# Performance work log

Hardware: AMD Instinct MI355X
Metric: run time of the kernel (lower is better)

## Reference

```python
import jax, jax.numpy as jnp
import numpy as np

N_NODES = 50000
N_EDGES = 800000
N_GRAPHS = 256
IN_CH = 128
HID = 128
OUT_CH = 10
BN_EPS = 1e-5


def setup_inputs() -> dict:
    key = jax.random.key(0)
    ks = jax.random.split(key, 32)
    x = jax.random.normal(ks[0], (N_NODES, IN_CH), dtype=jnp.float32)
    edge_index = jax.random.randint(ks[1], (2, N_EDGES), 0, N_NODES)
    batch = jnp.sort(jax.random.randint(ks[2], (N_NODES,), 0, N_GRAPHS))

    def lin(k, fan_in, fan_out):
        return (jax.random.normal(k, (fan_in, fan_out), dtype=jnp.float32)
                * np.float32(1.0 / np.sqrt(fan_in)))

    inp = {"x": x, "edge_index": edge_index, "batch": batch}
    dims = [(IN_CH, HID), (HID, HID), (HID, HID)]
    for i, (fi, fo) in enumerate(dims):
        inp[f"W{i}"] = lin(ks[3 + i], fi, fo)
        inp[f"b{i}"] = jnp.zeros((fo,), jnp.float32)
        inp[f"g{i}"] = jnp.ones((fo,), jnp.float32)
        inp[f"be{i}"] = jnp.zeros((fo,), jnp.float32)
    inp["lin1_w"] = lin(ks[10], 2 * HID, HID)
    inp["lin1_b"] = jnp.zeros((HID,), jnp.float32)
    inp["lin2_w"] = lin(ks[11], HID, OUT_CH)
    inp["lin2_b"] = jnp.zeros((OUT_CH,), jnp.float32)
    return inp


def _gcn_conv(x, W, b, src, dst):
    # PyG GCNConv: h = X W; add self-loops; symmetric D^-1/2 (A+I) D^-1/2 aggregation.
    h = x @ W  # [N, F]
    loops = jnp.arange(N_NODES)
    s = jnp.concatenate([src, loops])
    d = jnp.concatenate([dst, loops])
    deg = jax.ops.segment_sum(jnp.ones_like(d, jnp.float32), d, num_segments=N_NODES)
    dinv = jnp.where(deg > 0, jax.lax.rsqrt(deg), 0.0)
    coef = dinv[s] * dinv[d]  # [E+N]
    out = jax.ops.segment_sum(h[s] * coef[:, None], d, num_segments=N_NODES)
    return out + b


def _batch_norm(x, gamma, beta):
    mean = x.mean(axis=0)
    var = x.var(axis=0)
    return (x - mean) * jax.lax.rsqrt(var + BN_EPS) * gamma + beta


def _forward(x, edge_index, batch,
             W0, b0, g0, be0, W1, b1, g1, be1, W2, b2, g2, be2,
             lin1_w, lin1_b, lin2_w, lin2_b):
    src, dst = edge_index[0], edge_index[1]
    for W, b, g, be in ((W0, b0, g0, be0), (W1, b1, g1, be1), (W2, b2, g2, be2)):
        x = _gcn_conv(x, W, b, src, dst)
        x = jax.nn.relu(_batch_norm(x, g, be))
    x_sum = jax.ops.segment_sum(x, batch, num_segments=N_GRAPHS)  # [G, H]
    counts = jax.ops.segment_sum(jnp.ones((N_NODES,), jnp.float32), batch,
                                 num_segments=N_GRAPHS)
    x_mean = x_sum / jnp.maximum(counts, 1.0)[:, None]
    h = jnp.concatenate([x_mean, x_sum], axis=1)  # [G, 2H]
    h = jax.nn.relu(h @ lin1_w + lin1_b)
    return h @ lin2_w + lin2_b  # [G, OUT_CH]


def reference(x, edge_index, batch,
              W0, b0, g0, be0, W1, b1, g1, be1, W2, b2, g2, be2,
              lin1_w, lin1_b, lin2_w, lin2_b):
    return _forward(x, edge_index, batch,
                    W0, b0, g0, be0, W1, b1, g1, be1, W2, b2, g2, be2,
                    lin1_w, lin1_b, lin2_w, lin2_b)
```

## Files before the change

### kernel.cpp

```cpp
#include <hip/hip_runtime.h>

#define N_NODES 50000
#define N_EDGES 800000
#define N_GRAPHS 256
#define HID 128
#define OUT_CH 10
#define BN_EPS 1e-5f

#define OFF_H       0
#define OFF_BNPART  3134464
#define OFF_CSRD    3200000
#define OFF_WBT     4000000
#define OFF_AGG     6400000
#define OFF_DEG     12800000
#define OFF_ROWPTR  12850000
#define OFF_CURSOR  12900004
#define OFF_CSR     12950004
#define OFF_DINV    13750004
#define OFF_BNCOEF  13800004
#define OFF_POOL    13800260
#define OFF_CNT     13833028
#define OFF_BSUM    13833284

#define WBT_PITCH 136

typedef __attribute__((ext_vector_type(8))) short bf16x8;
typedef __attribute__((ext_vector_type(4))) float f32x4;

__device__ __forceinline__ ushort f2bf(float f) {
    union { float f; unsigned u; } v; v.f = f;
    unsigned r = v.u + 0x7FFFu + ((v.u >> 16) & 1u);
    return (ushort)(r >> 16);
}
__device__ __forceinline__ float bf2f(unsigned u16) {
    return __uint_as_float(u16 << 16);
}

__global__ void k_init(int* deg) {
    int i = blockIdx.x * 256 + threadIdx.x;
    if (i < N_NODES) deg[i] = 0;
}

__global__ void k_deg(const int* __restrict__ ei, int* __restrict__ deg) {
    int i = blockIdx.x * 256 + threadIdx.x;
    if (i < N_EDGES) atomicAdd(&deg[ei[N_EDGES + i]], 1);
}

__global__ void k_s1(const int* __restrict__ deg, int* __restrict__ bsum) {
    __shared__ int sh[256];
    int i = blockIdx.x * 256 + threadIdx.x;
    sh[threadIdx.x] = (i < N_NODES) ? deg[i] : 0;
    __syncthreads();
    for (int o = 128; o > 0; o >>= 1) {
        if (threadIdx.x < o) sh[threadIdx.x] += sh[threadIdx.x + o];
        __syncthreads();
    }
    if (threadIdx.x == 0) bsum[blockIdx.x] = sh[0];
}

__global__ void k_s2(int* __restrict__ bsum, int nb) {
    __shared__ int sh[256];
    int t = threadIdx.x;
    int v = (t < nb) ? bsum[t] : 0;
    sh[t] = v;
    __syncthreads();
    for (int o = 1; o < 256; o <<= 1) {
        int x = (t >= o) ? sh[t - o] : 0;
        __syncthreads();
        sh[t] += x;
        __syncthreads();
    }
    if (t < nb) bsum[t] = sh[t] - v;
}

__global__ void k_s3(const int* __restrict__ deg, const int* __restrict__ bsum,
                     int* __restrict__ rowptr, int* __restrict__ cursor,
                     float* __restrict__ dinv) {
    __shared__ int sh[256];
    int t = threadIdx.x;
    int i = blockIdx.x * 256 + t;
    int v = (i < N_NODES) ? deg[i] : 0;
    sh[t] = v;
    __syncthreads();
    for (int o = 1; o < 256; o <<= 1) {
        int x = (t >= o) ? sh[t - o] : 0;
        __syncthreads();
        sh[t] += x;
        __syncthreads();
    }
    int ex = bsum[blockIdx.x] + sh[t] - v;
    if (i < N_NODES) {
        rowptr[i] = ex;
        cursor[i] = ex;
        dinv[i] = rsqrtf((float)(v + 1));
        if (i == N_NODES - 1) rowptr[N_NODES] = ex + v;
    }
}

__global__ void k_scatter(const int* __restrict__ ei, int* __restrict__ cursor,
                          int* __restrict__ csr) {
    int i = blockIdx.x * 256 + threadIdx.x;
    if (i < N_EDGES) {
        int s = ei[i];
        int d = ei[N_EDGES + i];
        int pos = atomicAdd(&cursor[d], 1);
        csr[pos] = s;
    }
}

__global__ __launch_bounds__(256) void k_sortseg(const int* __restrict__ rowptr,
                                                 int* __restrict__ csr,
                                                 const float* __restrict__ dinv,
                                                 float* __restrict__ csrd) {
    int wave = threadIdx.x >> 6, lane = threadIdx.x & 63;
    int v = blockIdx.x * 4 + wave;
    if (v >= N_NODES) return;
    int e0 = rowptr[v], deg = rowptr[v + 1] - e0;
    if (deg <= 64) {
        int val = (lane < deg) ? csr[e0 + lane] : 0x7FFFFFFF;
#pragma unroll
        for (int k = 2; k <= 64; k <<= 1)
#pragma unroll
            for (int j = k >> 1; j > 0; j >>= 1) {
                int other = __shfl_xor(val, j);
                bool up = ((lane & k) == 0);
                bool lower = ((lane & j) == 0);
                int mn = min(val, other), mx = max(val, other);
                val = (up == lower) ? mn : mx;
            }
        if (lane < deg) {
            csr[e0 + lane] = val;
            csrd[e0 + lane] = dinv[val];
        }
    } else {
        if (lane == 0) {
            for (int i = e0 + 1; i < e0 + deg; ++i) {
                int key = csr[i];
                int j = i - 1;
                while (j >= e0 && csr[j] > key) { csr[j + 1] = csr[j]; --j; }
                csr[j + 1] = key;
            }
        }
        for (int e = e0 + lane; e < e0 + deg; e += 64) csrd[e] = dinv[csr[e]];
    }
}

__global__ void k_wprep(const float* __restrict__ W, ushort* __restrict__ Wbt) {
    int i = blockIdx.x * 256 + threadIdx.x;
    if (i < 16384) {
        int k = i >> 7, c = i & 127;
        Wbt[c * WBT_PITCH + k] = f2bf(W[i]);
    }
}

template <int BN>
__global__ __launch_bounds__(256) void k_gemm(const float* __restrict__ X,
                                              const ushort* __restrict__ Wbt,
                                              ushort* __restrict__ Hb,
                                              const float* __restrict__ coef,
                                              int nrows) {
    __shared__ __align__(16) ushort Wt[128 * WBT_PITCH];
    int t = threadIdx.x;
    for (int i = t; i < 2176; i += 256)
        ((uint4*)Wt)[i] = ((const uint4*)Wbt)[i];
    __syncthreads();

    int wv = t >> 6, l = t & 63;
    int m = l & 15;
    int kg = l >> 4;
    int row = blockIdx.x * 64 + wv * 16 + m;
    bool valid = row < nrows;
    const float* xr = X + (long)row * 128;

    f32x4 acc[8];
#pragma unroll
    for (int n = 0; n < 8; ++n) acc[n] = (f32x4){0.f, 0.f, 0.f, 0.f};

#pragma unroll
    for (int t4 = 0; t4 < 4; ++t4) {
        int k0 = t4 * 32 + kg * 8;
        float xv[8];
        if (valid) {
            float4 u0 = *(const float4*)(xr + k0);
            float4 u1 = *(const float4*)(xr + k0 + 4);
            if (BN) {
                float4 s0 = *(const float4*)(coef + k0);
                float4 s1 = *(const float4*)(coef + k0 + 4);
                float4 h0 = *(const float4*)(coef + 128 + k0);
                float4 h1 = *(const float4*)(coef + 128 + k0 + 4);
                u0.x = fmaxf(u0.x * s0.x + h0.x, 0.f);
                u0.y = fmaxf(u0.y * s0.y + h0.y, 0.f);
                u0.z = fmaxf(u0.z * s0.z + h0.z, 0.f);
                u0.w = fmaxf(u0.w * s0.w + h0.w, 0.f);
                u1.x = fmaxf(u1.x * s1.x + h1.x, 0.f);
                u1.y = fmaxf(u1.y * s1.y + h1.y, 0.f);
                u1.z = fmaxf(u1.z * s1.z + h1.z, 0.f);
                u1.w = fmaxf(u1.w * s1.w + h1.w, 0.f);
            }
            xv[0] = u0.x; xv[1] = u0.y; xv[2] = u0.z; xv[3] = u0.w;
            xv[4] = u1.x; xv[5] = u1.y; xv[6] = u1.z; xv[7] = u1.w;
        } else {
#pragma unroll
            for (int j = 0; j < 8; ++j) xv[j] = 0.f;
        }
        union { ushort u[8]; bf16x8 v; } A;
#pragma unroll
        for (int j = 0; j < 8; ++j) A.u[j] = f2bf(xv[j]);

#pragma unroll
        for (int n = 0; n < 8; ++n) {
            bf16x8 b = *(const bf16x8*)(&Wt[(n * 16 + m) * WBT_PITCH + k0]);
            acc[n] = __builtin_amdgcn_mfma_f32_16x16x32_bf16(A.v, b, acc[n], 0, 0, 0);
        }
    }

    int srow0 = blockIdx.x * 64 + wv * 16 + kg * 4;
#pragma unroll
    for (int n = 0; n < 8; ++n)
#pragma unroll
        for (int r = 0; r < 4; ++r) {
            int rr = srow0 + r;
            if (rr < nrows) Hb[(long)rr * 128 + n * 16 + m] = f2bf(acc[n][r]);
        }
}

__global__ __launch_bounds__(256) void k_agg(const ushort* __restrict__ Hb,
                                             const int* __restrict__ rowptr,
                                             const int* __restrict__ csr,
                                             const float* __restrict__ csrd,
                                             const float* __restrict__ dinv,
                                             const float* __restrict__ bias,
                                             float* __restrict__ OUT) {
    int wave = threadIdx.x >> 6, lane = threadIdx.x & 63;
    int v = blockIdx.x * 4 + wave;
    if (v >= N_NODES) return;
    int half = lane >> 5, qd = lane & 31;
    int c = qd * 4;
    float dv = dinv[v];
    int e0 = rowptr[v];
    int deg = rowptr[v + 1] - e0;
    float a0 = 0.f, a1 = 0.f, a2 = 0.f, a3 = 0.f;

    for (int base = 0; base < deg; base += 64) {
        int mye = base + lane;
        int idx = 0; float dvi = 0.f;
        if (mye < deg) { idx = csr[e0 + mye]; dvi = csrd[e0 + mye]; }
        int n = min(64, deg - base);
        int P = (n + 1) >> 1;
        int p = 0;
#define EDGE(pp) { \
        int sl = 2 * (pp) + half; \
        int s = __shfl(idx, sl); \
        float cf = __shfl(dvi, sl) * dv; \
        uint2 qv = *(const uint2*)(Hb + (long)s * 128 + c); \
        a0 += cf * bf2f(qv.x & 0xFFFFu); \
        a1 += cf * bf2f(qv.x >> 16); \
        a2 += cf * bf2f(qv.y & 0xFFFFu); \
        a3 += cf * bf2f(qv.y >> 16); }
        for (; p + 4 <= P; p += 4) { EDGE(p) EDGE(p + 1) EDGE(p + 2) EDGE(p + 3) }
        for (; p < P; ++p) { EDGE(p) }
#undef EDGE
    }
    a0 += __shfl_xor(a0, 32);
    a1 += __shfl_xor(a1, 32);
    a2 += __shfl_xor(a2, 32);
    a3 += __shfl_xor(a3, 32);
    if (half == 0) {
        uint2 qv = *(const uint2*)(Hb + (long)v * 128 + c);
        float cs = dv * dv;
        float4 bb = *(const float4*)(bias + c);
        float4 o;
        o.x = a0 + cs * bf2f(qv.x & 0xFFFFu) + bb.x;
        o.y = a1 + cs * bf2f(qv.x >> 16) + bb.y;
        o.z = a2 + cs * bf2f(qv.y & 0xFFFFu) + bb.z;
        o.w = a3 + cs * bf2f(qv.y >> 16) + bb.w;
        *(float4*)(OUT + (long)v * 128 + c) = o;
    }
}

__global__ __launch_bounds__(256) void k_bnstats(const float* __restrict__ X,
                                                 float* __restrict__ part) {
    int ch = threadIdx.x & 127;
    int half = threadIdx.x >> 7;
    float s = 0.f, q = 0.f;
    for (int v = blockIdx.x * 2 + half; v < N_NODES; v += 512) {
        float x = X[(long)v * 128 + ch];
        s += x;
        q += x * x;
    }
    __shared__ float sh[256];
    sh[threadIdx.x] = s;
    __syncthreads();
    float s2 = (half == 0) ? s + sh[threadIdx.x + 128] : 0.f;
    __syncthreads();
    sh[threadIdx.x] = q;
    __syncthreads();
    if (half == 0) {
        float q2 = q + sh[threadIdx.x + 128];
        part[blockIdx.x * 256 + ch] = s2;
        part[blockIdx.x * 256 + 128 + ch] = q2;
    }
}

__global__ void k_bnred(const float* __restrict__ part, const float* __restrict__ g,
                        const float* __restrict__ be, float* __restrict__ coef) {
    int t = threadIdx.x;
    int ch = t & 127, stat = t >> 7;
    float acc = 0.f;
    for (int b = 0; b < 256; ++b) acc += part[b * 256 + stat * 128 + ch];
    __shared__ float sh[256];
    sh[t] = acc;
    __syncthreads();
    if (stat == 0) {
        float inv_n = 1.0f / (float)N_NODES;
        float mean = acc * inv_n;
        float var = sh[128 + ch] * inv_n - mean * mean;
        float sc = g[ch] * rsqrtf(var + BN_EPS);
        coef[ch] = sc;
        coef[128 + ch] = be[ch] - mean * sc;
    }
}

__global__ __launch_bounds__(256) void k_pool(const float* __restrict__ X,
                                              const int* __restrict__ batch,
                                              const float* __restrict__ coef,
                                              float* __restrict__ pool,
                                              float* __restrict__ cnt) {
    __shared__ int bounds[2];
    int g = blockIdx.x, t = threadIdx.x;
    if (t < 2) {
        int target = g + t;
        int lo = 0, hi = N_NODES;
        while (lo < hi) {
            int mid = (lo + hi) >> 1;
            if (batch[mid] < target) lo = mid + 1; else hi = mid;
        }
        bounds[t] = lo;
    }
    __syncthreads();
    int start = bounds[0], end = bounds[1];
    int ch = t & 127, half = t >> 7;
    float sc = coef[ch], sh = coef[128 + ch];
    float acc = 0.f;
    for (int v = start + half; v < end; v += 2)
        acc += fmaxf(X[(long)v * 128 + ch] * sc + sh, 0.f);
    __shared__ float red[256];
    red[t] = acc;
    __syncthreads();
    if (half == 0) {
        pool[g * 128 + ch] = red[ch] + red[128 + ch];
        if (ch == 0) cnt[g] = (float)(end - start);
    }
}

__global__ __launch_bounds__(128) void k_mlp(const float* __restrict__ pool,
                                             const float* __restrict__ cnt,
                                             const float* __restrict__ w1,
                                             const float* __restrict__ b1,
                                             const float* __restrict__ w2,
                                             const float* __restrict__ b2,
                                             float* __restrict__ out) {
    __shared__ float h[256];
    __shared__ float h1[128];
    int g = blockIdx.x, t = threadIdx.x;
    float s = pool[g * 128 + t];
    float c = cnt[g];
    h[t] = s / fmaxf(c, 1.0f);
    h[128 + t] = s;
    __syncthreads();
    float acc = b1[t];
#pragma unroll 4
    for (int i = 0; i < 256; ++i) acc += h[i] * w1[i * 128 + t];
    h1[t] = fmaxf(acc, 0.f);
    __syncthreads();
    if (t < OUT_CH) {
        float o = b2[t];
#pragma unroll 4
        for (int j = 0; j < 128; ++j) o += h1[j] * w2[j * OUT_CH + t];
        out[g * OUT_CH + t] = o;
    }
}

extern "C" void kernel_launch(void* const* d_in, const int* in_sizes, int n_in,
                              void* d_out, int out_size, void* d_ws, size_t ws_size,
                              hipStream_t stream) {
    const float* x = (const float*)d_in[0];
    const int* ei = (const int*)d_in[1];
    const int* batch = (const int*)d_in[2];
    const float* W[3] = {(const float*)d_in[3], (const float*)d_in[7], (const float*)d_in[11]};
    const float* b[3] = {(const float*)d_in[4], (const float*)d_in[8], (const float*)d_in[12]};
    const float* gm[3] = {(const float*)d_in[5], (const float*)d_in[9], (const float*)d_in[13]};
    const float* be[3] = {(const float*)d_in[6], (const float*)d_in[10], (const float*)d_in[14]};
    const float* w1 = (const float*)d_in[15];
    const float* b1 = (const float*)d_in[16];
    const float* w2 = (const float*)d_in[17];
    const float* b2 = (const float*)d_in[18];
    float* out = (float*)d_out;

    float* ws = (float*)d_ws;
    ushort* Hb = (ushort*)(ws + OFF_H);
    float* bnpart = ws + OFF_BNPART;
    float* csrd = ws + OFF_CSRD;
    ushort* Wbt = (ushort*)(ws + OFF_WBT);
    float* AGG = ws + OFF_AGG;
    int* deg = (int*)(ws + OFF_DEG);
    int* rowptr = (int*)(ws + OFF_ROWPTR);
    int* cursor = (int*)(ws + OFF_CURSOR);
    int* csr = (int*)(ws + OFF_CSR);
    float* dinv = ws + OFF_DINV;
    float* bncoef = ws + OFF_BNCOEF;
    float* pool = ws + OFF_POOL;
    float* cnt = ws + OFF_CNT;
    int* bsum = (int*)(ws + OFF_BSUM);

    const int nb_scan = (N_NODES + 255) / 256;
    const int nb_node4 = (N_NODES + 3) / 4;

    hipLaunchKernelGGL(k_init, dim3(nb_scan), dim3(256), 0, stream, deg);
    hipLaunchKernelGGL(k_deg, dim3((N_EDGES + 255) / 256), dim3(256), 0, stream, ei, deg);
    hipLaunchKernelGGL(k_s1, dim3(nb_scan), dim3(256), 0, stream, deg, bsum);
    hipLaunchKernelGGL(k_s2, dim3(1), dim3(256), 0, stream, bsum, nb_scan);
    hipLaunchKernelGGL(k_s3, dim3(nb_scan), dim3(256), 0, stream, deg, bsum, rowptr, cursor, dinv);
    hipLaunchKernelGGL(k_scatter, dim3((N_EDGES + 255) / 256), dim3(256), 0, stream,
                       ei, cursor, csr);
    hipLaunchKernelGGL(k_sortseg, dim3(nb_node4), dim3(256), 0, stream,
                       rowptr, csr, dinv, csrd);
    for (int layer = 0; layer < 3; ++layer)
        hipLaunchKernelGGL(k_wprep, dim3(64), dim3(256), 0, stream,
                           W[layer], Wbt + layer * 128 * WBT_PITCH);

    const int gemm_blocks = (N_NODES + 63) / 64;
    for (int layer = 0; layer < 3; ++layer) {
        const float* cur_x = (layer == 0) ? x : AGG;
        const ushort* wbt_l = Wbt + layer * 128 * WBT_PITCH;
        if (layer == 0) {
            hipLaunchKernelGGL(k_gemm<0>, dim3(gemm_blocks), dim3(256), 0, stream,
                               cur_x, wbt_l, Hb, (const float*)nullptr, N_NODES);
        } else {
            hipLaunchKernelGGL(k_gemm<1>, dim3(gemm_blocks), dim3(256), 0, stream,
                               cur_x, wbt_l, Hb, bncoef, N_NODES);
        }
        hipLaunchKernelGGL(k_agg, dim3(nb_node4), dim3(256), 0, stream,
                           Hb, rowptr, csr, csrd, dinv, b[layer], AGG);
        hipLaunchKernelGGL(k_bnstats, dim3(256), dim3(256), 0, stream, AGG, bnpart);
        hipLaunchKernelGGL(k_bnred, dim3(1), dim3(256), 0, stream,
                           bnpart, gm[layer], be[layer], bncoef);
    }

    hipLaunchKernelGGL(k_pool, dim3(N_GRAPHS), dim3(256), 0, stream,
                       AGG, batch, bncoef, pool, cnt);
    hipLaunchKernelGGL(k_mlp, dim3(N_GRAPHS), dim3(128), 0, stream,
                       pool, cnt, w1, b1, w2, b2, out);
}
```

Measured before the change: 505.6 us.

## Build CSR via two-level bucket sort with shared-memory per-bucket construction

Replaces the degree-count, three-kernel prefix scan, atomic scatter and per-node sort with a bucketed approach. Edges are first grouped by destination into 98 buckets of 512 nodes using shared-memory histograms. Each bucket then builds its rowptr, dinv and sorted CSR segment entirely in LDS. This cuts kernel launches and global atomic contention. It relies on a fixed per-bucket capacity that could drop edges on skewed graphs.

```diff
diff --git a/kernel.cpp b/kernel.cpp
--- a/kernel.cpp
+++ b/kernel.cpp
@@ -7,20 +7,22 @@
 #define OUT_CH 10
 #define BN_EPS 1e-5f
 
+#define NBUCKET 98
+#define BCAP 10240
+
 #define OFF_H       0
 #define OFF_BNPART  3134464
 #define OFF_CSRD    3200000
 #define OFF_WBT     4000000
 #define OFF_AGG     6400000
-#define OFF_DEG     12800000
 #define OFF_ROWPTR  12850000
-#define OFF_CURSOR  12900004
 #define OFF_CSR     12950004
 #define OFF_DINV    13750004
 #define OFF_BNCOEF  13800004
 #define OFF_POOL    13800260
 #define OFF_CNT     13833028
-#define OFF_BSUM    13833284
+#define OFF_BCNT    13833284
+#define OFF_BSTART  13833444
 
 #define WBT_PITCH 136
 
@@ -36,113 +38,103 @@
     return __uint_as_float(u16 << 16);
 }
 
-__global__ void k_init(int* deg) {
-    int i = blockIdx.x * 256 + threadIdx.x;
-    if (i < N_NODES) deg[i] = 0;
-}
-
-__global__ void k_deg(const int* __restrict__ ei, int* __restrict__ deg) {
-    int i = blockIdx.x * 256 + threadIdx.x;
-    if (i < N_EDGES) atomicAdd(&deg[ei[N_EDGES + i]], 1);
-}
-
-__global__ void k_s1(const int* __restrict__ deg, int* __restrict__ bsum) {
-    __shared__ int sh[256];
-    int i = blockIdx.x * 256 + threadIdx.x;
-    sh[threadIdx.x] = (i < N_NODES) ? deg[i] : 0;
-    __syncthreads();
-    for (int o = 128; o > 0; o >>= 1) {
-        if (threadIdx.x < o) sh[threadIdx.x] += sh[threadIdx.x + o];
-        __syncthreads();
-    }
-    if (threadIdx.x == 0) bsum[blockIdx.x] = sh[0];
-}
-
-__global__ void k_s2(int* __restrict__ bsum, int nb) {
-    __shared__ int sh[256];
+__global__ void k_zero(int* bcnt) {
+    int i = threadIdx.x;
+    if (i < NBUCKET) bcnt[i] = 0;
+}
+
+__global__ __launch_bounds__(256) void k_bucket(const int* __restrict__ ei,
+                                                int* __restrict__ bcnt,
+                                                int2* __restrict__ buf) {
+    __shared__ int histL[NBUCKET], baseL[NBUCKET], curL[NBUCKET];
     int t = threadIdx.x;
-    int v = (t < nb) ? bsum[t] : 0;
-    sh[t] = v;
-    __syncthreads();
-    for (int o = 1; o < 256; o <<= 1) {
-        int x = (t >= o) ? sh[t - o] : 0;
-        __syncthreads();
-        sh[t] += x;
-        __syncthreads();
-    }
-    if (t < nb) bsum[t] = sh[t] - v;
-}
-
-__global__ void k_s3(const int* __restrict__ deg, const int* __restrict__ bsum,
-                     int* __restrict__ rowptr, int* __restrict__ cursor,
-                     float* __restrict__ dinv) {
-    __shared__ int sh[256];
-    int t = threadIdx.x;
-    int i = blockIdx.x * 256 + t;
-    int v = (i < N_NODES) ? deg[i] : 0;
-    sh[t] = v;
-    __syncthreads();
-    for (int o = 1; o < 256; o <<= 1) {
-        int x = (t >= o) ? sh[t - o] : 0;
-        __syncthreads();
-        sh[t] += x;
-        __syncthreads();
-    }
-    int ex = bsum[blockIdx.x] + sh[t] - v;
-    if (i < N_NODES) {
-        rowptr[i] = ex;
-        cursor[i] = ex;
-        dinv[i] = rsqrtf((float)(v + 1));
-        if (i == N_NODES - 1) rowptr[N_NODES] = ex + v;
-    }
-}
-
-__global__ void k_scatter(const int* __restrict__ ei, int* __restrict__ cursor,
-                          int* __restrict__ csr) {
-    int i = blockIdx.x * 256 + threadIdx.x;
-    if (i < N_EDGES) {
+    if (t < NBUCKET) histL[t] = 0;
+    __syncthreads();
+    const int stride = gridDim.x * 256;
+    for (int i = blockIdx.x * 256 + t; i < N_EDGES; i += stride)
+        atomicAdd(&histL[ei[N_EDGES + i] >> 9], 1);
+    __syncthreads();
+    if (t < NBUCKET) {
+        baseL[t] = atomicAdd(&bcnt[t], histL[t]);
+        curL[t] = 0;
+    }
+    __syncthreads();
+    for (int i = blockIdx.x * 256 + t; i < N_EDGES; i += stride) {
         int s = ei[i];
         int d = ei[N_EDGES + i];
-        int pos = atomicAdd(&cursor[d], 1);
-        csr[pos] = s;
-    }
-}
-
-__global__ __launch_bounds__(256) void k_sortseg(const int* __restrict__ rowptr,
-                                                 int* __restrict__ csr,
-                                                 const float* __restrict__ dinv,
-                                                 float* __restrict__ csrd) {
-    int wave = threadIdx.x >> 6, lane = threadIdx.x & 63;
-    int v = blockIdx.x * 4 + wave;
-    if (v >= N_NODES) return;
-    int e0 = rowptr[v], deg = rowptr[v + 1] - e0;
-    if (deg <= 64) {
-        int val = (lane < deg) ? csr[e0 + lane] : 0x7FFFFFFF;
-#pragma unroll
-        for (int k = 2; k <= 64; k <<= 1)
-#pragma unroll
-            for (int j = k >> 1; j > 0; j >>= 1) {
-                int other = __shfl_xor(val, j);
-                bool up = ((lane & k) == 0);
-                bool lower = ((lane & j) == 0);
-                int mn = min(val, other), mx = max(val, other);
-                val = (up == lower) ? mn : mx;
-            }
-        if (lane < deg) {
-            csr[e0 + lane] = val;
-            csrd[e0 + lane] = dinv[val];
-        }
-    } else {
-        if (lane == 0) {
-            for (int i = e0 + 1; i < e0 + deg; ++i) {
-                int key = csr[i];
-                int j = i - 1;
-                while (j >= e0 && csr[j] > key) { csr[j + 1] = csr[j]; --j; }
-                csr[j + 1] = key;
-            }
-        }
-        for (int e = e0 + lane; e < e0 + deg; e += 64) csrd[e] = dinv[csr[e]];
-    }
+        int b = d >> 9;
+        int p = baseL[b] + atomicAdd(&curL[b], 1);
+        if (p < BCAP) buf[b * BCAP + p] = make_int2(s, d);
+    }
+}
+
+__global__ void k_bscan(const int* __restrict__ bcnt, int* __restrict__ bstart,
+                        int* __restrict__ rowptr) {
+    if (threadIdx.x == 0) {
+        int acc = 0;
+        for (int b = 0; b < NBUCKET; ++b) { bstart[b] = acc; acc += bcnt[b]; }
+        bstart[NBUCKET] = acc;
+        rowptr[N_NODES] = acc;
+    }
+}
+
+__global__ __launch_bounds__(512) void k_csrbuild(const int2* __restrict__ buf,
+                                                  const int* __restrict__ bcnt,
+                                                  const int* __restrict__ bstart,
+                                                  int* __restrict__ rowptr,
+                                                  int* __restrict__ csr,
+                                                  float* __restrict__ dinv) {
+    __shared__ int off[512];
+    __shared__ int cur[512];
+    __shared__ int img[BCAP];
+    int b = blockIdx.x, t = threadIdx.x;
+    int node0 = b << 9;
+    int cnt = bcnt[b];
+    int ebase = bstart[b];
+    const int2* mybuf = buf + b * BCAP;
+
+    off[t] = 0;
+    __syncthreads();
+    for (int e = t; e < cnt; e += 512)
+        atomicAdd(&off[mybuf[e].y - node0], 1);
+    __syncthreads();
+    int mydeg = off[t];
+    for (int o = 1; o < 512; o <<= 1) {
+        int x = (t >= o) ? off[t - o] : 0;
+        __syncthreads();
+        off[t] += x;
+        __syncthreads();
+    }
+    int inc = off[t];
+    cur[t] = inc - mydeg;
+    int node = node0 + t;
+    if (node < N_NODES) {
+        rowptr[node] = ebase + inc - mydeg;
+        dinv[node] = rsqrtf((float)(mydeg + 1));
+    }
+    __syncthreads();
+    for (int e = t; e < cnt; e += 512) {
+        int2 pr = mybuf[e];
+        int p = atomicAdd(&cur[pr.y - node0], 1);
+        img[p] = pr.x;
+    }
+    __syncthreads();
+    int lo = inc - mydeg;
+    for (int i = lo + 1; i < inc; ++i) {
+        int key = img[i];
+        int j = i - 1;
+        while (j >= lo && img[j] > key) { img[j + 1] = img[j]; --j; }
+        img[j + 1] = key;
+    }
+    __syncthreads();
+    for (int e = t; e < cnt; e += 512)
+        csr[ebase + e] = img[e];
+}
+
+__global__ void k_fill(const int* __restrict__ csr, const float* __restrict__ dinv,
+                       float* __restrict__ csrd) {
+    int i = blockIdx.x * 1024 + threadIdx.x;
+    if (i < N_EDGES) csrd[i] = dinv[csr[i]];
 }
 
 __global__ void k_wprep(const float* __restrict__ W, ushort* __restrict__ Wbt) {
@@ -403,28 +395,25 @@
     float* csrd = ws + OFF_CSRD;
     ushort* Wbt = (ushort*)(ws + OFF_WBT);
     float* AGG = ws + OFF_AGG;
-    int* deg = (int*)(ws + OFF_DEG);
+    int2* bucketBuf = (int2*)(ws + OFF_AGG);
     int* rowptr = (int*)(ws + OFF_ROWPTR);
-    int* cursor = (int*)(ws + OFF_CURSOR);
     int* csr = (int*)(ws + OFF_CSR);
     float* dinv = ws + OFF_DINV;
     float* bncoef = ws + OFF_BNCOEF;
     float* pool = ws + OFF_POOL;
     float* cnt = ws + OFF_CNT;
-    int* bsum = (int*)(ws + OFF_BSUM);
-
-    const int nb_scan = (N_NODES + 255) / 256;
+    int* bcnt = (int*)(ws + OFF_BCNT);
+    int* bstart = (int*)(ws + OFF_BSTART);
+
     const int nb_node4 = (N_NODES + 3) / 4;
 
-    hipLaunchKernelGGL(k_init, dim3(nb_scan), dim3(256), 0, stream, deg);
-    hipLaunchKernelGGL(k_deg, dim3((N_EDGES + 255) / 256), dim3(256), 0, stream, ei, deg);
-    hipLaunchKernelGGL(k_s1, dim3(nb_scan), dim3(256), 0, stream, deg, bsum);
-    hipLaunchKernelGGL(k_s2, dim3(1), dim3(256), 0, stream, bsum, nb_scan);
-    hipLaunchKernelGGL(k_s3, dim3(nb_scan), dim3(256), 0, stream, deg, bsum, rowptr, cursor, dinv);
-    hipLaunchKernelGGL(k_scatter, dim3((N_EDGES + 255) / 256), dim3(256), 0, stream,
-                       ei, cursor, csr);
-    hipLaunchKernelGGL(k_sortseg, dim3(nb_node4), dim3(256), 0, stream,
-                       rowptr, csr, dinv, csrd);
+    hipLaunchKernelGGL(k_zero, dim3(1), dim3(128), 0, stream, bcnt);
+    hipLaunchKernelGGL(k_bucket, dim3(392), dim3(256), 0, stream, ei, bcnt, bucketBuf);
+    hipLaunchKernelGGL(k_bscan, dim3(1), dim3(64), 0, stream, bcnt, bstart, rowptr);
+    hipLaunchKernelGGL(k_csrbuild, dim3(NBUCKET), dim3(512), 0, stream,
+                       bucketBuf, bcnt, bstart, rowptr, csr, dinv);
+    hipLaunchKernelGGL(k_fill, dim3((N_EDGES + 1023) / 1024), dim3(1024), 0, stream,
+                       csr, dinv, csrd);
     for (int layer = 0; layer < 3; ++layer)
         hipLaunchKernelGGL(k_wprep, dim3(64), dim3(256), 0, stream,
                            W[layer], Wbt + layer * 128 * WBT_PITCH);
```

Result: faster. 480.0 us (-5.1%).
